# Kernel tuning notes

Measured on AMD Instinct MI355X. Metric: run time of the kernel, lower is better.

Reference implementation:

```python
import jax, jax.numpy as jnp
import numpy as np

B, P, N, H = 2, 512, 8, 32
INIT_RANGE = 0.02


def setup_inputs() -> dict:
    key = jax.random.key(0)
    k1, k2, k3 = jax.random.split(key, 3)
    d = jax.random.normal(k1, (B, P, N, H), dtype=jnp.float32)
    e = jax.random.normal(k2, (B, P, N, H), dtype=jnp.float32)
    W = jax.random.normal(k3, (N, H, H, H), dtype=jnp.float32) * INIT_RANGE
    return {"d": d, "e": e, "W": W}


def reference(d, e, W):
    # Trilinear contraction: v[b,p1,p2,n,h3] = sum_{h1,h2} d[b,p1,n,h1] e[b,p2,n,h2] W[n,h1,h2,h3]
    # Decompose into two batched matmuls to avoid the naive 4-way product:
    # tmp[b,p1,n,h2,h3] = sum_h1 d[b,p1,n,h1] W[n,h1,h2,h3]
    tmp = jnp.einsum('bpni,nijk->bpnjk', d, W)
    # v[b,p1,p2,n,h3] = sum_h2 tmp[b,p1,n,h2,h3] e[b,p2,n,h2]
    v = jnp.einsum('bpnjk,bqnj->bpqnk', tmp, e)
    return v
```

## Files before the change

kernel.cpp:

```cpp
#include <hip/hip_runtime.h>

#define BB 2
#define PP 512
#define NN 8
#define HH 32

typedef float f4     __attribute__((ext_vector_type(4)));
typedef float f32x4  __attribute__((ext_vector_type(4)));
typedef short bf16x8 __attribute__((ext_vector_type(8)));

__device__ __forceinline__ short f2bf(float f) {
  union { float f; unsigned u; } v; v.f = f;
  unsigned r = v.u + 0x7FFFu + ((v.u >> 16) & 1u);
  return (short)(r >> 16);
}

__global__ __launch_bounds__(256) void prep_all_kernel(
    const float* __restrict__ d, const float* __restrict__ W,
    const float* __restrict__ e, short* __restrict__ tmpT,
    short* __restrict__ eBf) {
  const int bid = blockIdx.x;
  const int t   = threadIdx.x;

  if (bid >= 512) {
    const int ft = (bid - 512) * 256 + t;
    const int l  = ft & 63;
    const int n  = (ft >> 6) & 7;
    const int pt = (ft >> 9) & 31;
    const int b  = ft >> 14;
    const float* src =
        e + (((size_t)(b * PP + pt * 16 + (l & 15)) * NN + n) * HH + (l >> 4) * 8);
    const f4 e0 = *(const f4*)src;
    const f4 e1 = *(const f4*)(src + 4);
    bf16x8 v;
    v[0] = f2bf(e0[0]); v[1] = f2bf(e0[1]); v[2] = f2bf(e0[2]); v[3] = f2bf(e0[3]);
    v[4] = f2bf(e1[0]); v[5] = f2bf(e1[1]); v[6] = f2bf(e1[2]); v[7] = f2bf(e1[3]);
    *(bf16x8*)(eBf + (size_t)ft * 8) = v;
    return;
  }

  const int b      = bid >> 8;
  const int rem    = bid & 255;
  const int npair  = rem >> 6;
  const int p1base = (rem & 63) * 8;

  __shared__ float dsh[2][32][8];
  {
    const int h1 = t & 31, p1l = (t >> 5) & 7;
    #pragma unroll
    for (int r = 0; r < 2; ++r)
      dsh[r][h1][p1l] =
          d[(size_t)((b * PP + p1base + p1l) * NN + npair * 2 + r) * HH + h1];
  }
  __syncthreads();

  const int np  = t >> 7;
  const int h3  = (t >> 2) & 31;
  const int h2g = t & 3;
  const int n   = npair * 2 + np;

  float acc[8][8];
  #pragma unroll
  for (int p = 0; p < 8; ++p)
    #pragma unroll
    for (int q = 0; q < 8; ++q) acc[p][q] = 0.f;

  const float* wb = W + (size_t)n * 32768 + h2g * 8 * 32 + h3;
  for (int h1 = 0; h1 < 32; ++h1) {
    const float* wr = wb + (size_t)h1 * 1024;
    float wq[8];
    #pragma unroll
    for (int q = 0; q < 8; ++q) wq[q] = wr[q * 32];
    const f4 d0 = *(const f4*)&dsh[np][h1][0];
    const f4 d1 = *(const f4*)&dsh[np][h1][4];
    #pragma unroll
    for (int p = 0; p < 4; ++p) {
      #pragma unroll
      for (int q = 0; q < 4; ++q) {
        acc[p][q]         = fmaf(d0[p], wq[q],     acc[p][q]);
        acc[p][q + 4]     = fmaf(d0[p], wq[q + 4], acc[p][q + 4]);
        acc[p + 4][q]     = fmaf(d1[p], wq[q],     acc[p + 4][q]);
        acc[p + 4][q + 4] = fmaf(d1[p], wq[q + 4], acc[p + 4][q + 4]);
      }
    }
  }

  const size_t obase =
      ((size_t)(b * PP + p1base) * NN + n) * (HH * HH) + h3 * 32 + h2g * 8;
  #pragma unroll
  for (int p = 0; p < 8; ++p) {
    bf16x8 v;
    #pragma unroll
    for (int q = 0; q < 8; ++q) v[q] = f2bf(acc[p][q]);
    *(bf16x8*)(tmpT + obase + (size_t)p * (NN * HH * HH)) = v;
  }
}

__global__ __launch_bounds__(256, 4) void vmain_kernel(
    const short* __restrict__ eBf, const short* __restrict__ tmpT,
    float* __restrict__ out) {
  const int bid = blockIdx.x;
  const int b   = bid >> 9;
  const int p1  = bid & 511;
  const int t   = threadIdx.x;
  const int wv  = t >> 6;
  const int l   = t & 63;
  const int lr  = l & 15;
  const int lk  = l >> 4;

  __shared__ float lbuf[4][16][128];
  float* wl = &lbuf[wv][0][0];

  bf16x8 bfr[8][2];
  const short* tb = tmpT + (size_t)(b * PP + p1) * (NN * HH * HH);
  #pragma unroll
  for (int n = 0; n < 8; ++n)
    #pragma unroll
    for (int c = 0; c < 2; ++c)
      bfr[n][c] = *(const bf16x8*)(tb + n * (HH * HH) + (c * 16 + lr) * 32 + lk * 8);

  const short* eb   = eBf + (size_t)b * (32 * NN * 512);
  float*       outb = out + (size_t)(b * PP + p1) * (PP * NN * HH);
  const f32x4  z    = {0.f, 0.f, 0.f, 0.f};

  for (int i = 0; i < 8; ++i) {
    const int pt = wv * 8 + i;
    const int m0 = pt * 16;
    #pragma unroll
    for (int half = 0; half < 2; ++half) {
      const int n0 = half * 4;
      #pragma unroll
      for (int nn = 0; nn < 4; ++nn) {
        const int n = n0 + nn;
        const bf16x8 a =
            *(const bf16x8*)(eb + (((size_t)(pt * NN + n)) << 9) + l * 8);
        const f32x4 c0 = __builtin_amdgcn_mfma_f32_16x16x32_bf16(bfr[n][0], a, z, 0, 0, 0);
        const f32x4 c1 = __builtin_amdgcn_mfma_f32_16x16x32_bf16(bfr[n][1], a, z, 0, 0, 0);
        const int s0 = (nn * 8 + lk)     ^ (lr & 7);
        const int s1 = (nn * 8 + 4 + lk) ^ (lr & 7);
        *(f32x4*)(wl + lr * 128 + s0 * 4) = c0;
        *(f32x4*)(wl + lr * 128 + s1 * 4) = c1;
      }
      #pragma unroll
      for (int j = 0; j < 8; ++j) {
        const int row  = 2 * j + (l >> 5);
        const int slot = l & 31;
        const f32x4 v = *(const f32x4*)(wl + row * 128 + ((slot ^ (row & 7)) * 4));
        *(f32x4*)(outb + (size_t)(m0 + row) * (NN * HH) + n0 * HH + slot * 4) = v;
      }
    }
  }
}

__global__ __launch_bounds__(256, 4) void fused_kernel(
    const float* __restrict__ d, const float* __restrict__ e,
    const float* __restrict__ W, float* __restrict__ out) {
  const int bid = blockIdx.x;
  const int b   = bid >> 9;
  const int p1  = bid & 511;
  const int t   = threadIdx.x;

  __shared__ float dsh[NN * HH];
  __shared__ short tsh[NN * HH * HH];
  dsh[t] = d[(size_t)(b * PP + p1) * (NN * HH) + t];
  __syncthreads();

  const int h3  = t & 31;
  const int h2b = t >> 5;
  for (int n = 0; n < 8; ++n) {
    f4 dv[8];
    #pragma unroll
    for (int j = 0; j < 8; ++j) dv[j] = *(const f4*)&dsh[n * 32 + j * 4];
    const float* Wn = W + (size_t)n * (HH * HH * HH);
    #pragma unroll
    for (int h2s = 0; h2s < 4; ++h2s) {
      const int h2 = h2s * 8 + h2b;
      float acc = 0.f;
      #pragma unroll
      for (int j = 0; j < 8; ++j)
        #pragma unroll
        for (int k = 0; k < 4; ++k)
          acc = fmaf(dv[j][k], Wn[(j * 4 + k) * 1024 + h2 * 32 + h3], acc);
      tsh[n * 1024 + h3 * 32 + h2] = f2bf(acc);
    }
  }
  __syncthreads();

  const int wv = t >> 6;
  const int l  = t & 63;
  const int lr = l & 15;
  const int lk = l >> 4;
  bf16x8 bfr[8][2];
  #pragma unroll
  for (int n = 0; n < 8; ++n)
    #pragma unroll
    for (int c = 0; c < 2; ++c)
      bfr[n][c] = *(const bf16x8*)&tsh[n * (HH * HH) + (c * 16 + lr) * 32 + lk * 8];

  const float* eb   = e + (size_t)b * (PP * NN * HH);
  float*       outb = out + (size_t)(b * PP + p1) * (PP * NN * HH);
  const f32x4  z    = {0.f, 0.f, 0.f, 0.f};
  for (int i = 0; i < 8; ++i) {
    const int m0 = (wv * 8 + i) * 16;
    #pragma unroll
    for (int n = 0; n < 8; ++n) {
      const float* ep = eb + (size_t)(((m0 + lr) * NN + n) * HH + lk * 8);
      const f4 e0 = *(const f4*)ep;
      const f4 e1 = *(const f4*)(ep + 4);
      bf16x8 a;
      a[0] = f2bf(e0[0]); a[1] = f2bf(e0[1]); a[2] = f2bf(e0[2]); a[3] = f2bf(e0[3]);
      a[4] = f2bf(e1[0]); a[5] = f2bf(e1[1]); a[6] = f2bf(e1[2]); a[7] = f2bf(e1[3]);
      const f32x4 c0 = __builtin_amdgcn_mfma_f32_16x16x32_bf16(bfr[n][0], a, z, 0, 0, 0);
      const f32x4 c1 = __builtin_amdgcn_mfma_f32_16x16x32_bf16(bfr[n][1], a, z, 0, 0, 0);
      float* op = outb + (size_t)(m0 + lr) * (NN * HH) + n * HH + lk * 4;
      *(f32x4*)op        = c0;
      *(f32x4*)(op + 16) = c1;
    }
  }
}

extern "C" void kernel_launch(void* const* d_in, const int* in_sizes, int n_in,
                              void* d_out, int out_size, void* d_ws, size_t ws_size,
                              hipStream_t stream) {
  const float* d = (const float*)d_in[0];
  const float* e = (const float*)d_in[1];
  const float* W = (const float*)d_in[2];
  float* out = (float*)d_out;

  const size_t tmp_bytes = (size_t)BB * PP * NN * HH * HH * sizeof(short);
  const size_t eb_bytes  = (size_t)BB * PP * NN * HH * sizeof(short);
  if (ws_size >= tmp_bytes + eb_bytes) {
    short* tmpT = (short*)d_ws;
    short* eBf  = (short*)((char*)d_ws + tmp_bytes);
    prep_all_kernel<<<dim3(512 + 128), dim3(256), 0, stream>>>(d, W, e, tmpT, eBf);
    vmain_kernel<<<dim3(BB * PP), dim3(256), 0, stream>>>(eBf, tmpT, out);
  } else {
    fused_kernel<<<dim3(BB * PP), dim3(256), 0, stream>>>(d, e, W, out);
  }
}
```

Before: 132.3 us.

## Split heads across waves and write full 1KB output rows via shared staging

Each wave in vmain_kernel now owns two heads for all 512 p2 rows instead of all eight heads for a slice of p2. Results from the four waves are staged in a double-buffered shared tile so each wave can store complete contiguous 256-float output rows. The aim is longer, fully coalesced global stores and fewer B-fragment registers, which should help occupancy. The cost is a block-wide barrier on every one of the 32 iterations.

After: 126.9 us. 1.04x faster.

```diff
diff --git a/kernel.cpp b/kernel.cpp
--- a/kernel.cpp
+++ b/kernel.cpp
@@ -107,47 +107,42 @@
   const int l   = t & 63;
   const int lr  = l & 15;
   const int lk  = l >> 4;
-
-  __shared__ float lbuf[4][16][128];
-  float* wl = &lbuf[wv][0][0];
-
-  bf16x8 bfr[8][2];
+  const int n0w = wv * 2;
+
+  __shared__ float sh[2][16][256];
+
+  bf16x8 bfr[2][2];
   const short* tb = tmpT + (size_t)(b * PP + p1) * (NN * HH * HH);
   #pragma unroll
-  for (int n = 0; n < 8; ++n)
+  for (int s = 0; s < 2; ++s)
     #pragma unroll
     for (int c = 0; c < 2; ++c)
-      bfr[n][c] = *(const bf16x8*)(tb + n * (HH * HH) + (c * 16 + lr) * 32 + lk * 8);
+      bfr[s][c] =
+          *(const bf16x8*)(tb + (n0w + s) * 1024 + (c * 16 + lr) * 32 + lk * 8);
 
   const short* eb   = eBf + (size_t)b * (32 * NN * 512);
   float*       outb = out + (size_t)(b * PP + p1) * (PP * NN * HH);
   const f32x4  z    = {0.f, 0.f, 0.f, 0.f};
 
-  for (int i = 0; i < 8; ++i) {
-    const int pt = wv * 8 + i;
-    const int m0 = pt * 16;
-    #pragma unroll
-    for (int half = 0; half < 2; ++half) {
-      const int n0 = half * 4;
-      #pragma unroll
-      for (int nn = 0; nn < 4; ++nn) {
-        const int n = n0 + nn;
-        const bf16x8 a =
-            *(const bf16x8*)(eb + (((size_t)(pt * NN + n)) << 9) + l * 8);
-        const f32x4 c0 = __builtin_amdgcn_mfma_f32_16x16x32_bf16(bfr[n][0], a, z, 0, 0, 0);
-        const f32x4 c1 = __builtin_amdgcn_mfma_f32_16x16x32_bf16(bfr[n][1], a, z, 0, 0, 0);
-        const int s0 = (nn * 8 + lk)     ^ (lr & 7);
-        const int s1 = (nn * 8 + 4 + lk) ^ (lr & 7);
-        *(f32x4*)(wl + lr * 128 + s0 * 4) = c0;
-        *(f32x4*)(wl + lr * 128 + s1 * 4) = c1;
-      }
-      #pragma unroll
-      for (int j = 0; j < 8; ++j) {
-        const int row  = 2 * j + (l >> 5);
-        const int slot = l & 31;
-        const f32x4 v = *(const f32x4*)(wl + row * 128 + ((slot ^ (row & 7)) * 4));
-        *(f32x4*)(outb + (size_t)(m0 + row) * (NN * HH) + n0 * HH + slot * 4) = v;
-      }
+  for (int i = 0; i < 32; ++i) {
+    const int bi = i & 1;
+    #pragma unroll
+    for (int s = 0; s < 2; ++s) {
+      const int n = n0w + s;
+      const bf16x8 a = *(const bf16x8*)(eb + (((size_t)(i * NN + n)) << 9) + l * 8);
+      const f32x4 c0 = __builtin_amdgcn_mfma_f32_16x16x32_bf16(bfr[s][0], a, z, 0, 0, 0);
+      const f32x4 c1 = __builtin_amdgcn_mfma_f32_16x16x32_bf16(bfr[s][1], a, z, 0, 0, 0);
+      const int g0 = (n * 8 + lk)     ^ (lr & 7);
+      const int g1 = (n * 8 + 4 + lk) ^ (lr & 7);
+      *(f32x4*)(&sh[bi][lr][g0 * 4]) = c0;
+      *(f32x4*)(&sh[bi][lr][g1 * 4]) = c1;
+    }
+    __syncthreads();
+    #pragma unroll
+    for (int k = 0; k < 4; ++k) {
+      const int r = wv * 4 + k;
+      const f32x4 v = *(const f32x4*)(&sh[bi][r][((l ^ (r & 7)) * 4)]);
+      *(f32x4*)(outb + (size_t)(i * 16 + r) * 256 + l * 4) = v;
     }
   }
 }
```
